# Kernel tuning notes

Measured on AMD Instinct MI355X. Metric: run time of the kernel, lower is better.

## Reference

```python
import jax, jax.numpy as jnp
import numpy as np

N = 1048576
B = 1024
H = 128
EPS = 1e-12  # F.normalize default eps


def setup_inputs() -> dict:
    key = jax.random.key(0)
    k1, k2, k3 = jax.random.split(key, 3)
    emb = jax.random.normal(k1, (N, H), dtype=jnp.float32)
    summary = jax.random.normal(k2, (B, H), dtype=jnp.float32)
    # CSR-style ptr: 0 = ptr[0] <= ... <= ptr[B] = N
    inner = jnp.sort(jax.random.randint(k3, (B - 1,), 0, N))
    ptr = jnp.concatenate([jnp.zeros((1,), jnp.int64),
                           inner.astype(jnp.int64),
                           jnp.full((1,), N, jnp.int64)])
    d = jnp.ones((H,), dtype=jnp.float32)
    scale = jnp.ones((1,), dtype=jnp.float32)
    return {"emb": emb, "summary": summary, "ptr": ptr, "d": d, "scale": scale}


def reference(emb, summary, ptr, d, scale):
    # L2-normalize each row (torch F.normalize: x / max(||x||, eps))
    norm = jnp.linalg.norm(emb, axis=-1, keepdims=True)
    emb_n = emb / jnp.maximum(norm, EPS)
    # node -> graph segment id from ptr (node i belongs to segment s iff ptr[s] <= i < ptr[s+1])
    seg = jnp.searchsorted(ptr[1:], jnp.arange(emb.shape[0]), side="right")  # [N]
    # fused diag-scale + per-graph ragged dot: out[n] = sum_h emb_n[n,h] * d[h] * summary[seg[n],h]
    s_per_node = summary[seg]  # [N, H] gather
    sim = jnp.sum(emb_n * d[None, :] * s_per_node, axis=-1)  # [N]
    return sim * scale[0]
```

## Files before the change

### kernel.cpp

```cpp
#include <hip/hip_runtime.h>
#include <math.h>


#define HDIM 128
#define NEPS 1e-12f

__global__ void seg_fill(const int* __restrict__ ptr, int* __restrict__ seg) {
    const int s  = blockIdx.x;
    const int lo = ptr[s], hi = ptr[s + 1];
    for (int i = lo + threadIdx.x; i < hi; i += blockDim.x)
        seg[i] = s;
}

__global__ void sd_fill(const float* __restrict__ summary,
                        const float* __restrict__ dvec,
                        const float* __restrict__ scale,
                        float* __restrict__ sd, int total) {
    const int i = blockIdx.x * blockDim.x + threadIdx.x;
    if (i < total) sd[i] = summary[i] * dvec[i & (HDIM - 1)] * scale[0];
}

__global__ __launch_bounds__(256) void sim_main(
    const float* __restrict__ emb,
    const float* __restrict__ sd,
    const int* __restrict__ seg,
    float* __restrict__ out, int N)
{
    const int tid = blockIdx.x * blockDim.x + threadIdx.x;
    const int sub = tid & 7;
    const long long row = (long long)(tid >> 3);
    if (row >= N) return;

    const int s = seg[row];
    const float4* e4 = (const float4*)(emb + row * (long long)HDIM);
    const float4* w4 = (const float4*)(sd + (long long)s * HDIM);

    float sumsq = 0.f, dot = 0.f;
    #pragma unroll
    for (int j = 0; j < 4; ++j) {
        const float4 e = e4[sub + 8 * j];
        const float4 w = w4[sub + 8 * j];
        sumsq = fmaf(e.x, e.x, sumsq); sumsq = fmaf(e.y, e.y, sumsq);
        sumsq = fmaf(e.z, e.z, sumsq); sumsq = fmaf(e.w, e.w, sumsq);
        dot   = fmaf(e.x, w.x, dot);   dot   = fmaf(e.y, w.y, dot);
        dot   = fmaf(e.z, w.z, dot);   dot   = fmaf(e.w, w.w, dot);
    }
    #pragma unroll
    for (int m = 4; m >= 1; m >>= 1) {
        sumsq += __shfl_xor(sumsq, m, 64);
        dot   += __shfl_xor(dot,   m, 64);
    }
    if (sub == 0)
        out[row] = dot / fmaxf(sqrtf(sumsq), NEPS);
}

__global__ __launch_bounds__(256) void sim_fallback(
    const float* __restrict__ emb, const float* __restrict__ summary,
    const int* __restrict__ ptr, const float* __restrict__ dvec,
    const float* __restrict__ scale, float* __restrict__ out, int N, int B)
{
    const int tid  = blockIdx.x * blockDim.x + threadIdx.x;
    const int lane = tid & 63;
    const int half = lane >> 5;
    const int l    = lane & 31;
    const long long row = (long long)(tid >> 6) * 2 + half;
    if (row >= N) return;
    int lo = 0, hi = B;
    while (lo < hi) {
        int mid = (lo + hi) >> 1;
        if (ptr[1 + mid] <= (int)row) lo = mid + 1; else hi = mid;
    }
    const float4* e4 = (const float4*)(emb + row * HDIM);
    const float4* s4 = (const float4*)(summary + (long long)lo * HDIM);
    const float4* d4 = (const float4*)dvec;
    const float4 e = e4[l], s = s4[l], dd = d4[l];
    float sumsq = e.x*e.x + e.y*e.y + e.z*e.z + e.w*e.w;
    float dot   = e.x*dd.x*s.x + e.y*dd.y*s.y + e.z*dd.z*s.z + e.w*dd.w*s.w;
    #pragma unroll
    for (int m = 16; m >= 1; m >>= 1) {
        sumsq += __shfl_xor(sumsq, m, 64);
        dot   += __shfl_xor(dot,   m, 64);
    }
    if (l == 0)
        out[row] = dot / fmaxf(sqrtf(sumsq), NEPS) * scale[0];
}

extern "C" void kernel_launch(void* const* d_in, const int* in_sizes, int n_in,
                              void* d_out, int out_size, void* d_ws, size_t ws_size,
                              hipStream_t stream) {
    const float* emb     = (const float*)d_in[0];
    const float* summary = (const float*)d_in[1];
    const int*   ptr     = (const int*)d_in[2];
    const float* dvec    = (const float*)d_in[3];
    const float* scale   = (const float*)d_in[4];
    float*       out     = (float*)d_out;

    const int Hn = in_sizes[3];
    const int N  = in_sizes[0] / Hn;
    const int B  = in_sizes[1] / Hn;

    const size_t sd_bytes  = (size_t)B * Hn * sizeof(float);
    const size_t seg_bytes = (size_t)N * sizeof(int);

    if (ws_size >= sd_bytes + seg_bytes) {
        float* sd  = (float*)d_ws;
        int*   seg = (int*)((char*)d_ws + sd_bytes);

        seg_fill<<<B, 256, 0, stream>>>(ptr, seg);
        const int sd_total = B * Hn;
        sd_fill<<<(sd_total + 255) / 256, 256, 0, stream>>>(summary, dvec,
                                                            scale, sd, sd_total);
        sim_main<<<(N + 31) / 32, 256, 0, stream>>>(emb, sd, seg, out, N);
    } else {
        sim_fallback<<<(N + 7) / 8, 256, 0, stream>>>(emb, summary, ptr, dvec,
                                                      scale, out, N, B);
    }
}
```

Measured before the change: 679.9 us.

## Fuse prep kernels and process two rows per thread group in sim_main

Merges the segment-fill and scaled-summary kernels into one prep kernel, which removes a launch. The main kernel now handles two rows per 8-lane group, 16 rows per wave, so each thread has more loads in flight. The shuffle reductions are packed into 64-bit shuffles that carry two floats each. The kernel is bound by emb reads (512MB), so the launch savings and extra memory-level parallelism are small, and the extra registers could lower occupancy.

```diff
diff --git a/kernel.cpp b/kernel.cpp
--- a/kernel.cpp
+++ b/kernel.cpp
@@ -5,19 +5,25 @@
 #define HDIM 128
 #define NEPS 1e-12f
 
-__global__ void seg_fill(const int* __restrict__ ptr, int* __restrict__ seg) {
+__global__ void prep(const int* __restrict__ ptr,
+                     const float* __restrict__ summary,
+                     const float* __restrict__ dvec,
+                     const float* __restrict__ scale,
+                     float* __restrict__ sd, int* __restrict__ seg) {
     const int s  = blockIdx.x;
+    const float sc = scale[0];
+    for (int h = threadIdx.x; h < HDIM; h += blockDim.x)
+        sd[s * HDIM + h] = summary[s * HDIM + h] * dvec[h] * sc;
     const int lo = ptr[s], hi = ptr[s + 1];
     for (int i = lo + threadIdx.x; i < hi; i += blockDim.x)
         seg[i] = s;
 }
 
-__global__ void sd_fill(const float* __restrict__ summary,
-                        const float* __restrict__ dvec,
-                        const float* __restrict__ scale,
-                        float* __restrict__ sd, int total) {
-    const int i = blockIdx.x * blockDim.x + threadIdx.x;
-    if (i < total) sd[i] = summary[i] * dvec[i & (HDIM - 1)] * scale[0];
+__device__ inline float2 shfl_xor_f2(float2 v, int m) {
+    union { double d; float2 f; } u;
+    u.f = v;
+    u.d = __shfl_xor(u.d, m, 64);
+    return u.f;
 }
 
 __global__ __launch_bounds__(256) void sim_main(
@@ -26,32 +32,62 @@
     const int* __restrict__ seg,
     float* __restrict__ out, int N)
 {
-    const int tid = blockIdx.x * blockDim.x + threadIdx.x;
-    const int sub = tid & 7;
-    const long long row = (long long)(tid >> 3);
-    if (row >= N) return;
+    const int tid  = blockIdx.x * blockDim.x + threadIdx.x;
+    const int lane = tid & 63;
+    const int sub  = lane & 7;
+    const int grp  = lane >> 3;
+    const long long wave = (long long)(tid >> 6);
 
-    const int s = seg[row];
-    const float4* e4 = (const float4*)(emb + row * (long long)HDIM);
-    const float4* w4 = (const float4*)(sd + (long long)s * HDIM);
+    const long long r0 = wave * 16 + grp;
+    const long long r1 = r0 + 8;
+    if (r0 >= N) return;
+    const bool has1 = (r1 < N);
 
-    float sumsq = 0.f, dot = 0.f;
+    const int s0 = seg[r0];
+    const int s1 = has1 ? seg[r1] : s0;
+
+    const float4* e0 = (const float4*)(emb + r0 * HDIM);
+    const float4* e1 = (const float4*)(emb + r1 * HDIM);
+    const float4* w0 = (const float4*)(sd + (long long)s0 * HDIM);
+    const float4* w1 = (const float4*)(sd + (long long)s1 * HDIM);
+
+    float2 acc0 = {0.f, 0.f};
+    float2 acc1 = {0.f, 0.f};
+
     #pragma unroll
     for (int j = 0; j < 4; ++j) {
-        const float4 e = e4[sub + 8 * j];
-        const float4 w = w4[sub + 8 * j];
-        sumsq = fmaf(e.x, e.x, sumsq); sumsq = fmaf(e.y, e.y, sumsq);
-        sumsq = fmaf(e.z, e.z, sumsq); sumsq = fmaf(e.w, e.w, sumsq);
-        dot   = fmaf(e.x, w.x, dot);   dot   = fmaf(e.y, w.y, dot);
-        dot   = fmaf(e.z, w.z, dot);   dot   = fmaf(e.w, w.w, dot);
+        const float4 a = e0[sub + 8 * j];
+        const float4 b = w0[sub + 8 * j];
+        acc0.x = fmaf(a.x, b.x, acc0.x); acc0.y = fmaf(a.x, a.x, acc0.y);
+        acc0.x = fmaf(a.y, b.y, acc0.x); acc0.y = fmaf(a.y, a.y, acc0.y);
+        acc0.x = fmaf(a.z, b.z, acc0.x); acc0.y = fmaf(a.z, a.z, acc0.y);
+        acc0.x = fmaf(a.w, b.w, acc0.x); acc0.y = fmaf(a.w, a.w, acc0.y);
     }
+    if (has1) {
+        #pragma unroll
+        for (int j = 0; j < 4; ++j) {
+            const float4 a = e1[sub + 8 * j];
+            const float4 b = w1[sub + 8 * j];
+            acc1.x = fmaf(a.x, b.x, acc1.x); acc1.y = fmaf(a.x, a.x, acc1.y);
+            acc1.x = fmaf(a.y, b.y, acc1.x); acc1.y = fmaf(a.y, a.y, acc1.y);
+            acc1.x = fmaf(a.z, b.z, acc1.x); acc1.y = fmaf(a.z, a.z, acc1.y);
+            acc1.x = fmaf(a.w, b.w, acc1.x); acc1.y = fmaf(a.w, a.w, acc1.y);
+        }
+    }
+
     #pragma unroll
     for (int m = 4; m >= 1; m >>= 1) {
-        sumsq += __shfl_xor(sumsq, m, 64);
-        dot   += __shfl_xor(dot,   m, 64);
+        const float2 o0 = shfl_xor_f2(acc0, m);
+        const float2 o1 = shfl_xor_f2(acc1, m);
+        acc0.x += o0.x; acc0.y += o0.y;
+        acc1.x += o1.x; acc1.y += o1.y;
     }
-    if (sub == 0)
-        out[row] = dot / fmaxf(sqrtf(sumsq), NEPS);
+
+    if (sub == 0) {
+        out[r0] = acc0.x / fmaxf(sqrtf(acc0.y), NEPS);
+        if (has1)
+            out[r1] = acc1.x / fmaxf(sqrtf(acc1.y), NEPS);
+    }
 }
 
 __global__ __launch_bounds__(256) void sim_fallback(
@@ -106,11 +142,8 @@
         float* sd  = (float*)d_ws;
         int*   seg = (int*)((char*)d_ws + sd_bytes);
 
-        seg_fill<<<B, 256, 0, stream>>>(ptr, seg);
-        const int sd_total = B * Hn;
-        sd_fill<<<(sd_total + 255) / 256, 256, 0, stream>>>(summary, dvec,
-                                                            scale, sd, sd_total);
-        sim_main<<<(N + 31) / 32, 256, 0, stream>>>(emb, sd, seg, out, N);
+        prep<<<B, 256, 0, stream>>>(ptr, summary, dvec, scale, sd, seg);
+        sim_main<<<(N + 63) / 64, 256, 0, stream>>>(emb, sd, seg, out, N);
     } else {
         sim_fallback<<<(N + 7) / 8, 256, 0, stream>>>(emb, summary, ptr, dvec,
                                                       scale, out, N, B);
```

After: 682.5 us. Within noise of the previous version (+0.4%).
